# Performance work log

Measured on AMD Instinct MI355X. Metric: run time of the kernel, lower is better.

Reference implementation:

```python
import jax, jax.numpy as jnp
import numpy as np


def setup_inputs() -> dict:
    key = jax.random.key(0)
    k1, k2 = jax.random.split(key)
    B, S = 128, 131072
    x = jax.random.normal(k1, (B, S), dtype=jnp.float32)
    mask = jax.random.randint(k2, (B, S), 0, 2).astype(jnp.bool_)
    return {"x": x, "mask": mask}


def reference(x, mask):
    # Masked cumulative sum along dim=1: fused mask-multiply + prefix scan.
    return jnp.cumsum(x * mask.astype(x.dtype), axis=1)
```

## Files before the change

kernel.cpp:

```cpp
#include <hip/hip_runtime.h>


#define TPB 512
#define B_ROWS 128
#define S_LEN 131072
#define TILE 16384
#define TPR 8
#define NBLK 512
#define NWAVE 8
#define MAGIC 0x7F3A9C51u

typedef float f32x4 __attribute__((ext_vector_type(4)));

#define UNPACK_PR(rd, XV, MW)                                          \
    pr[rd][0] = (XV).x * (float)((MW) & 0xffu);                        \
    pr[rd][1] = pr[rd][0] + (XV).y * (float)(((MW) >> 8) & 0xffu);     \
    pr[rd][2] = pr[rd][1] + (XV).z * (float)(((MW) >> 16) & 0xffu);    \
    pr[rd][3] = pr[rd][2] + (XV).w * (float)((MW) >> 24);

#define MUL_PR_I(rd, XV, MI)                                           \
    pr[rd][0] = (XV).x * (float)(MI).x;                                \
    pr[rd][1] = pr[rd][0] + (XV).y * (float)(MI).y;                    \
    pr[rd][2] = pr[rd][1] + (XV).z * (float)(MI).z;                    \
    pr[rd][3] = pr[rd][2] + (XV).w * (float)(MI).w;

__device__ __forceinline__ void lds_barrier() {
    asm volatile("s_waitcnt lgkmcnt(0)" ::: "memory");
    __builtin_amdgcn_s_barrier();
}

__global__ void __launch_bounds__(TPB, 2)
mscan(const float* __restrict__ x, const void* __restrict__ mask,
      float* __restrict__ out, unsigned* __restrict__ ticket,
      unsigned long long* __restrict__ desc) {
    __shared__ unsigned s_vb;
    __shared__ float wtA[NWAVE], wtB[NWAVE];
    __shared__ float s_prevA;

    const int t = threadIdx.x;
    const int lane = t & 63, wid = t >> 6;

    if (t == 0) s_vb = atomicAdd(ticket, 1u) & (NBLK - 1);
    __syncthreads();
    const unsigned vb = s_vb;
    const int r = vb >> 2, q = vb & 3;
    const int tidA = r * TPR + 2 * q;
    const long eA = (long)r * S_LEN + (long)(2 * q) * TILE;
    const long eB = eA + TILE;

    const char* xbA  = (const char*)x + eA * 4 + wid * 8192 + lane * 16;
    const char* xbA2 = xbA + 4096;
    const char* mbA  = (const char*)mask + eA + wid * 2048 + lane * 4;
    const char* xbB  = (const char*)x + eB * 4 + wid * 8192 + lane * 16;
    const char* xbB2 = xbB + 4096;
    const char* mbB  = (const char*)mask + eB + wid * 2048 + lane * 4;
    const unsigned* dwp = (const unsigned*)mask + lane;

    unsigned dw;
    f32x4 x0, x1, x2, x3, x4v, x5, x6, x7;
    unsigned m0, m1, m2, m3, m4, m5, m6, m7;
    asm volatile(
        "global_load_dword %0, %17, off\n\t"
        "global_load_dwordx4 %1, %18, off\n\t"
        "global_load_dwordx4 %2, %18, off offset:1024\n\t"
        "global_load_dwordx4 %3, %18, off offset:2048\n\t"
        "global_load_dwordx4 %4, %18, off offset:3072\n\t"
        "global_load_dwordx4 %5, %19, off\n\t"
        "global_load_dwordx4 %6, %19, off offset:1024\n\t"
        "global_load_dwordx4 %7, %19, off offset:2048\n\t"
        "global_load_dwordx4 %8, %19, off offset:3072\n\t"
        "global_load_dword %9, %20, off\n\t"
        "global_load_dword %10, %20, off offset:256\n\t"
        "global_load_dword %11, %20, off offset:512\n\t"
        "global_load_dword %12, %20, off offset:768\n\t"
        "global_load_dword %13, %20, off offset:1024\n\t"
        "global_load_dword %14, %20, off offset:1280\n\t"
        "global_load_dword %15, %20, off offset:1536\n\t"
        "global_load_dword %16, %20, off offset:1792\n\t"
        "s_waitcnt vmcnt(0)"
        : "=&v"(dw), "=&v"(x0), "=&v"(x1), "=&v"(x2), "=&v"(x3),
          "=&v"(x4v), "=&v"(x5), "=&v"(x6), "=&v"(x7),
          "=&v"(m0), "=&v"(m1), "=&v"(m2), "=&v"(m3),
          "=&v"(m4), "=&v"(m5), "=&v"(m6), "=&v"(m7)
        : "v"(dwp), "v"(xbA), "v"(xbA2), "v"(mbA)
        : "memory");

    const bool m_i32 = (__all(dw <= 1u) != 0);

    float pr[8][4];
    f32x4 y0, y1, y2, y3, y4, y5, y6, y7;
    unsigned n0, n1, n2, n3, n4, n5, n6, n7;
    if (!m_i32) {
        UNPACK_PR(0, x0, m0)  UNPACK_PR(1, x1, m1)
        UNPACK_PR(2, x2, m2)  UNPACK_PR(3, x3, m3)
        UNPACK_PR(4, x4v, m4) UNPACK_PR(5, x5, m5)
        UNPACK_PR(6, x6, m6)  UNPACK_PR(7, x7, m7)
        asm volatile(
            "global_load_dwordx4 %0, %16, off\n\t"
            "global_load_dwordx4 %1, %16, off offset:1024\n\t"
            "global_load_dwordx4 %2, %16, off offset:2048\n\t"
            "global_load_dwordx4 %3, %16, off offset:3072\n\t"
            "global_load_dwordx4 %4, %17, off\n\t"
            "global_load_dwordx4 %5, %17, off offset:1024\n\t"
            "global_load_dwordx4 %6, %17, off offset:2048\n\t"
            "global_load_dwordx4 %7, %17, off offset:3072\n\t"
            "global_load_dword %8, %18, off\n\t"
            "global_load_dword %9, %18, off offset:256\n\t"
            "global_load_dword %10, %18, off offset:512\n\t"
            "global_load_dword %11, %18, off offset:768\n\t"
            "global_load_dword %12, %18, off offset:1024\n\t"
            "global_load_dword %13, %18, off offset:1280\n\t"
            "global_load_dword %14, %18, off offset:1536\n\t"
            "global_load_dword %15, %18, off offset:1792"
            : "=&v"(y0), "=&v"(y1), "=&v"(y2), "=&v"(y3),
              "=&v"(y4), "=&v"(y5), "=&v"(y6), "=&v"(y7),
              "=&v"(n0), "=&v"(n1), "=&v"(n2), "=&v"(n3),
              "=&v"(n4), "=&v"(n5), "=&v"(n6), "=&v"(n7)
            : "v"(xbB), "v"(xbB2), "v"(mbB)
            : "memory");
    } else {
        const char* mibA = (const char*)mask + eA * 4 + wid * 8192 + lane * 16;
        const int4 a0 = *(const int4*)(mibA + 0 * 1024);
        const int4 a1 = *(const int4*)(mibA + 1 * 1024);
        const int4 a2 = *(const int4*)(mibA + 2 * 1024);
        const int4 a3 = *(const int4*)(mibA + 3 * 1024);
        const int4 a4 = *(const int4*)(mibA + 4 * 1024);
        const int4 a5 = *(const int4*)(mibA + 5 * 1024);
        const int4 a6 = *(const int4*)(mibA + 6 * 1024);
        const int4 a7 = *(const int4*)(mibA + 7 * 1024);
        MUL_PR_I(0, x0, a0)  MUL_PR_I(1, x1, a1)
        MUL_PR_I(2, x2, a2)  MUL_PR_I(3, x3, a3)
        MUL_PR_I(4, x4v, a4) MUL_PR_I(5, x5, a5)
        MUL_PR_I(6, x6, a6)  MUL_PR_I(7, x7, a7)
    }

    float incA[8], rtA[8];
    #pragma unroll
    for (int rd = 0; rd < 8; ++rd) {
        float vv = pr[rd][3];
        #pragma unroll
        for (int off = 1; off < 64; off <<= 1) {
            const float n = __shfl_up(vv, off, 64);
            if (lane >= off) vv += n;
        }
        incA[rd] = vv;
        rtA[rd] = __shfl(vv, 63, 64);
    }
    float wsumA = 0.0f;
    #pragma unroll
    for (int rd = 0; rd < 8; ++rd) wsumA += rtA[rd];
    if (lane == 0) wtA[wid] = wsumA;
    lds_barrier();

    float wpreA = 0.0f, TA = 0.0f;
    #pragma unroll
    for (int w = 0; w < NWAVE; ++w) {
        const float qv = wtA[w];
        if (w < wid) wpreA += qv;
        TA += qv;
    }

    if (t == 0) {
        float prev = 0.0f;
        if (q != 0) {
            const unsigned long long* dp = &desc[tidA - 1];
            unsigned long long d;
            while (((d = __hip_atomic_load(dp, __ATOMIC_RELAXED,
                                           __HIP_MEMORY_SCOPE_AGENT)) >> 32)
                   != (unsigned long long)MAGIC)
                __builtin_amdgcn_s_sleep(2);
            union { unsigned u; float f; } cv; cv.u = (unsigned)d; prev = cv.f;
        }
        union { float f; unsigned u; } tv; tv.f = prev + TA;
        __hip_atomic_store(&desc[tidA],
                           ((unsigned long long)MAGIC << 32) | tv.u,
                           __ATOMIC_RELAXED, __HIP_MEMORY_SCOPE_AGENT);
        s_prevA = prev;
    }
    lds_barrier();
    const float prevA = s_prevA;

    {
        const float baseA = prevA + wpreA;
        char* ob = (char*)out + eA * 4 + wid * 8192 + lane * 16;
        float rpre = 0.0f;
        #pragma unroll
        for (int rd = 0; rd < 8; ++rd) {
            const float excl = baseA + rpre + (incA[rd] - pr[rd][3]);
            f32x4 ov;
            ov.x = excl + pr[rd][0];
            ov.y = excl + pr[rd][1];
            ov.z = excl + pr[rd][2];
            ov.w = excl + pr[rd][3];
            __builtin_nontemporal_store(ov, (f32x4*)(ob + rd * 1024));
            rpre += rtA[rd];
        }
    }

    if (!m_i32) {
        asm volatile("s_waitcnt vmcnt(8)" ::: "memory");
        __builtin_amdgcn_sched_barrier(0);
        UNPACK_PR(0, y0, n0)  UNPACK_PR(1, y1, n1)
        UNPACK_PR(2, y2, n2)  UNPACK_PR(3, y3, n3)
        UNPACK_PR(4, y4, n4)  UNPACK_PR(5, y5, n5)
        UNPACK_PR(6, y6, n6)  UNPACK_PR(7, y7, n7)
    } else {
        asm volatile("s_waitcnt vmcnt(0)" ::: "memory");
        __builtin_amdgcn_sched_barrier(0);
        const char* xib = (const char*)x + eB * 4 + wid * 8192 + lane * 16;
        const char* mib = (const char*)mask + eB * 4 + wid * 8192 + lane * 16;
        #pragma unroll
        for (int rd = 0; rd < 8; ++rd) {
            const f32x4 xv = *(const f32x4*)(xib + rd * 1024);
            const int4 mv = *(const int4*)(mib + rd * 1024);
            MUL_PR_I(rd, xv, mv)
        }
    }

    float incB[8], rtB[8];
    #pragma unroll
    for (int rd = 0; rd < 8; ++rd) {
        float vv = pr[rd][3];
        #pragma unroll
        for (int off = 1; off < 64; off <<= 1) {
            const float n = __shfl_up(vv, off, 64);
            if (lane >= off) vv += n;
        }
        incB[rd] = vv;
        rtB[rd] = __shfl(vv, 63, 64);
    }
    float wsumB = 0.0f;
    #pragma unroll
    for (int rd = 0; rd < 8; ++rd) wsumB += rtB[rd];
    if (lane == 0) wtB[wid] = wsumB;
    lds_barrier();

    float wpreB = 0.0f, TB = 0.0f;
    #pragma unroll
    for (int w = 0; w < NWAVE; ++w) {
        const float qv = wtB[w];
        if (w < wid) wpreB += qv;
        TB += qv;
    }
    const float prevB = prevA + TA;

    if (t == 0) {
        union { float f; unsigned u; } tv; tv.f = prevB + TB;
        __hip_atomic_store(&desc[tidA + 1],
                           ((unsigned long long)MAGIC << 32) | tv.u,
                           __ATOMIC_RELAXED, __HIP_MEMORY_SCOPE_AGENT);
    }

    {
        const float baseB = prevB + wpreB;
        char* ob = (char*)out + eB * 4 + wid * 8192 + lane * 16;
        float rpre = 0.0f;
        #pragma unroll
        for (int rd = 0; rd < 8; ++rd) {
            const float excl = baseB + rpre + (incB[rd] - pr[rd][3]);
            f32x4 ov;
            ov.x = excl + pr[rd][0];
            ov.y = excl + pr[rd][1];
            ov.z = excl + pr[rd][2];
            ov.w = excl + pr[rd][3];
            __builtin_nontemporal_store(ov, (f32x4*)(ob + rd * 1024));
            rpre += rtB[rd];
        }
    }
}

extern "C" void kernel_launch(void* const* d_in, const int* in_sizes, int n_in,
                              void* d_out, int out_size, void* d_ws, size_t ws_size,
                              hipStream_t stream) {
    const float* x    = (const float*)d_in[0];
    const void*  mask = d_in[1];
    float*       out  = (float*)d_out;

    unsigned* ticket         = (unsigned*)d_ws;
    unsigned long long* desc = (unsigned long long*)((char*)d_ws + 256);

    mscan<<<NBLK, TPB, 0, stream>>>(x, mask, out, ticket, desc);
}
```

Baseline: 41.08 us.

## Split each row into two 1024-thread blocks and hoist all tile loads upfront

Reorganizes the decoupled-lookback scan so each row is covered by two blocks of 1024 threads (256 blocks total) instead of four 512-thread blocks. Both sub-tiles' loads for x and the byte mask are now issued before any compute, rather than the second tile's loads waiting on the first. The lookback chain per row becomes a single dependency. The second-half block must wait for the first half's full total before storing anything, so more work sits on a serial dependency. Fewer blocks also lowers available parallelism and wave occupancy per CU.

After: 48.56 us. 1.18x slower.

```diff
diff --git a/kernel.cpp b/kernel.cpp
--- a/kernel.cpp
+++ b/kernel.cpp
@@ -1,13 +1,12 @@
 #include <hip/hip_runtime.h>
 
 
-#define TPB 512
+#define TPB 1024
+#define NWAVE 16
 #define B_ROWS 128
 #define S_LEN 131072
-#define TILE 16384
-#define TPR 8
-#define NBLK 512
-#define NWAVE 8
+#define SUB 32768
+#define NBLK 256
 #define MAGIC 0x7F3A9C51u
 
 typedef float f32x4 __attribute__((ext_vector_type(4)));
@@ -29,13 +28,49 @@
     __builtin_amdgcn_s_barrier();
 }
 
-__global__ void __launch_bounds__(TPB, 2)
+__device__ __forceinline__ float wave_scan8(const float (&pr)[8][4],
+                                            float (&inc)[8], float (&rt)[8],
+                                            const int lane) {
+    float tot = 0.0f;
+    #pragma unroll
+    for (int rd = 0; rd < 8; ++rd) {
+        float vv = pr[rd][3];
+        #pragma unroll
+        for (int off = 1; off < 64; off <<= 1) {
+            const float n = __shfl_up(vv, off, 64);
+            if (lane >= off) vv += n;
+        }
+        inc[rd] = vv;
+        rt[rd] = __shfl(vv, 63, 64);
+        tot += rt[rd];
+    }
+    return tot;
+}
+
+__device__ __forceinline__ void store8(const float (&pr)[8][4],
+                                       const float (&inc)[8], const float (&rt)[8],
+                                       const float base, char* ob) {
+    float rpre = 0.0f;
+    #pragma unroll
+    for (int rd = 0; rd < 8; ++rd) {
+        const float excl = base + rpre + (inc[rd] - pr[rd][3]);
+        f32x4 ov;
+        ov.x = excl + pr[rd][0];
+        ov.y = excl + pr[rd][1];
+        ov.z = excl + pr[rd][2];
+        ov.w = excl + pr[rd][3];
+        __builtin_nontemporal_store(ov, (f32x4*)(ob + rd * 1024));
+        rpre += rt[rd];
+    }
+}
+
+__global__ void __launch_bounds__(TPB)
 mscan(const float* __restrict__ x, const void* __restrict__ mask,
       float* __restrict__ out, unsigned* __restrict__ ticket,
       unsigned long long* __restrict__ desc) {
     __shared__ unsigned s_vb;
-    __shared__ float wtA[NWAVE], wtB[NWAVE];
-    __shared__ float s_prevA;
+    __shared__ float wt[NWAVE];
+    __shared__ float s_prev;
 
     const int t = threadIdx.x;
     const int lane = t & 63, wid = t >> 6;
@@ -43,17 +78,21 @@
     if (t == 0) s_vb = atomicAdd(ticket, 1u) & (NBLK - 1);
     __syncthreads();
     const unsigned vb = s_vb;
-    const int r = vb >> 2, q = vb & 3;
-    const int tidA = r * TPR + 2 * q;
-    const long eA = (long)r * S_LEN + (long)(2 * q) * TILE;
-    const long eB = eA + TILE;
-
-    const char* xbA  = (const char*)x + eA * 4 + wid * 8192 + lane * 16;
+    const int h = vb >> 7;
+    const int r = vb & (B_ROWS - 1);
+    const long eA = (long)r * S_LEN + (long)h * (2 * SUB);
+    const long eB = eA + SUB;
+
+    const int xoff = wid * 8192 + lane * 16;
+    const int moff = wid * 2048 + lane * 4;
+    const char* xw = (const char*)x;
+    const char* mw = (const char*)mask;
+    const char* xbA  = xw + eA * 4 + xoff;
     const char* xbA2 = xbA + 4096;
-    const char* mbA  = (const char*)mask + eA + wid * 2048 + lane * 4;
-    const char* xbB  = (const char*)x + eB * 4 + wid * 8192 + lane * 16;
+    const char* mbA  = mw + eA + moff;
+    const char* xbB  = xw + eB * 4 + xoff;
     const char* xbB2 = xbB + 4096;
-    const char* mbB  = (const char*)mask + eB + wid * 2048 + lane * 4;
+    const char* mbB  = mw + eB + moff;
     const unsigned* dwp = (const unsigned*)mask + lane;
 
     unsigned dw;
@@ -76,8 +115,7 @@
         "global_load_dword %13, %20, off offset:1024\n\t"
         "global_load_dword %14, %20, off offset:1280\n\t"
         "global_load_dword %15, %20, off offset:1536\n\t"
-        "global_load_dword %16, %20, off offset:1792\n\t"
-        "s_waitcnt vmcnt(0)"
+        "global_load_dword %16, %20, off offset:1792"
         : "=&v"(dw), "=&v"(x0), "=&v"(x1), "=&v"(x2), "=&v"(x3),
           "=&v"(x4v), "=&v"(x5), "=&v"(x6), "=&v"(x7),
           "=&v"(m0), "=&v"(m1), "=&v"(m2), "=&v"(m3),
@@ -85,85 +123,70 @@
         : "v"(dwp), "v"(xbA), "v"(xbA2), "v"(mbA)
         : "memory");
 
-    const bool m_i32 = (__all(dw <= 1u) != 0);
-
-    float pr[8][4];
     f32x4 y0, y1, y2, y3, y4, y5, y6, y7;
     unsigned n0, n1, n2, n3, n4, n5, n6, n7;
+    asm volatile(
+        "global_load_dwordx4 %0, %16, off\n\t"
+        "global_load_dwordx4 %1, %16, off offset:1024\n\t"
+        "global_load_dwordx4 %2, %16, off offset:2048\n\t"
+        "global_load_dwordx4 %3, %16, off offset:3072\n\t"
+        "global_load_dwordx4 %4, %17, off\n\t"
+        "global_load_dwordx4 %5, %17, off offset:1024\n\t"
+        "global_load_dwordx4 %6, %17, off offset:2048\n\t"
+        "global_load_dwordx4 %7, %17, off offset:3072\n\t"
+        "global_load_dword %8, %18, off\n\t"
+        "global_load_dword %9, %18, off offset:256\n\t"
+        "global_load_dword %10, %18, off offset:512\n\t"
+        "global_load_dword %11, %18, off offset:768\n\t"
+        "global_load_dword %12, %18, off offset:1024\n\t"
+        "global_load_dword %13, %18, off offset:1280\n\t"
+        "global_load_dword %14, %18, off offset:1536\n\t"
+        "global_load_dword %15, %18, off offset:1792"
+        : "=&v"(y0), "=&v"(y1), "=&v"(y2), "=&v"(y3),
+          "=&v"(y4), "=&v"(y5), "=&v"(y6), "=&v"(y7),
+          "=&v"(n0), "=&v"(n1), "=&v"(n2), "=&v"(n3),
+          "=&v"(n4), "=&v"(n5), "=&v"(n6), "=&v"(n7)
+        : "v"(xbB), "v"(xbB2), "v"(mbB)
+        : "memory");
+
+    asm volatile("s_waitcnt vmcnt(16)" ::: "memory");
+    __builtin_amdgcn_sched_barrier(0);
+    const bool m_i32 = (__all(dw <= 1u) != 0);
+
+    float pr[8][4];
     if (!m_i32) {
         UNPACK_PR(0, x0, m0)  UNPACK_PR(1, x1, m1)
         UNPACK_PR(2, x2, m2)  UNPACK_PR(3, x3, m3)
         UNPACK_PR(4, x4v, m4) UNPACK_PR(5, x5, m5)
         UNPACK_PR(6, x6, m6)  UNPACK_PR(7, x7, m7)
-        asm volatile(
-            "global_load_dwordx4 %0, %16, off\n\t"
-            "global_load_dwordx4 %1, %16, off offset:1024\n\t"
-            "global_load_dwordx4 %2, %16, off offset:2048\n\t"
-            "global_load_dwordx4 %3, %16, off offset:3072\n\t"
-            "global_load_dwordx4 %4, %17, off\n\t"
-            "global_load_dwordx4 %5, %17, off offset:1024\n\t"
-            "global_load_dwordx4 %6, %17, off offset:2048\n\t"
-            "global_load_dwordx4 %7, %17, off offset:3072\n\t"
-            "global_load_dword %8, %18, off\n\t"
-            "global_load_dword %9, %18, off offset:256\n\t"
-            "global_load_dword %10, %18, off offset:512\n\t"
-            "global_load_dword %11, %18, off offset:768\n\t"
-            "global_load_dword %12, %18, off offset:1024\n\t"
-            "global_load_dword %13, %18, off offset:1280\n\t"
-            "global_load_dword %14, %18, off offset:1536\n\t"
-            "global_load_dword %15, %18, off offset:1792"
-            : "=&v"(y0), "=&v"(y1), "=&v"(y2), "=&v"(y3),
-              "=&v"(y4), "=&v"(y5), "=&v"(y6), "=&v"(y7),
-              "=&v"(n0), "=&v"(n1), "=&v"(n2), "=&v"(n3),
-              "=&v"(n4), "=&v"(n5), "=&v"(n6), "=&v"(n7)
-            : "v"(xbB), "v"(xbB2), "v"(mbB)
-            : "memory");
     } else {
-        const char* mibA = (const char*)mask + eA * 4 + wid * 8192 + lane * 16;
-        const int4 a0 = *(const int4*)(mibA + 0 * 1024);
-        const int4 a1 = *(const int4*)(mibA + 1 * 1024);
-        const int4 a2 = *(const int4*)(mibA + 2 * 1024);
-        const int4 a3 = *(const int4*)(mibA + 3 * 1024);
-        const int4 a4 = *(const int4*)(mibA + 4 * 1024);
-        const int4 a5 = *(const int4*)(mibA + 5 * 1024);
-        const int4 a6 = *(const int4*)(mibA + 6 * 1024);
-        const int4 a7 = *(const int4*)(mibA + 7 * 1024);
-        MUL_PR_I(0, x0, a0)  MUL_PR_I(1, x1, a1)
-        MUL_PR_I(2, x2, a2)  MUL_PR_I(3, x3, a3)
-        MUL_PR_I(4, x4v, a4) MUL_PR_I(5, x5, a5)
-        MUL_PR_I(6, x6, a6)  MUL_PR_I(7, x7, a7)
-    }
-
-    float incA[8], rtA[8];
-    #pragma unroll
-    for (int rd = 0; rd < 8; ++rd) {
-        float vv = pr[rd][3];
+        asm volatile("s_waitcnt vmcnt(0)" ::: "memory");
+        __builtin_amdgcn_sched_barrier(0);
+        const char* mib = mw + eA * 4 + xoff;
         #pragma unroll
-        for (int off = 1; off < 64; off <<= 1) {
-            const float n = __shfl_up(vv, off, 64);
-            if (lane >= off) vv += n;
-        }
-        incA[rd] = vv;
-        rtA[rd] = __shfl(vv, 63, 64);
-    }
-    float wsumA = 0.0f;
-    #pragma unroll
-    for (int rd = 0; rd < 8; ++rd) wsumA += rtA[rd];
-    if (lane == 0) wtA[wid] = wsumA;
-    lds_barrier();
-
+        for (int rd = 0; rd < 8; ++rd) {
+            const f32x4 xv = *(const f32x4*)(xw + eA * 4 + xoff + rd * 1024);
+            const int4 mv = *(const int4*)(mib + rd * 1024);
+            MUL_PR_I(rd, xv, mv)
+        }
+    }
+
+    float inc[8], rt[8];
+    const float wavetotA = wave_scan8(pr, inc, rt, lane);
+    if (lane == 0) wt[wid] = wavetotA;
+    lds_barrier();
     float wpreA = 0.0f, TA = 0.0f;
     #pragma unroll
     for (int w = 0; w < NWAVE; ++w) {
-        const float qv = wtA[w];
+        const float qv = wt[w];
         if (w < wid) wpreA += qv;
         TA += qv;
     }
 
     if (t == 0) {
         float prev = 0.0f;
-        if (q != 0) {
-            const unsigned long long* dp = &desc[tidA - 1];
+        if (h != 0) {
+            const unsigned long long* dp = &desc[r];
             unsigned long long d;
             while (((d = __hip_atomic_load(dp, __ATOMIC_RELAXED,
                                            __HIP_MEMORY_SCOPE_AGENT)) >> 32)
@@ -171,31 +194,12 @@
                 __builtin_amdgcn_s_sleep(2);
             union { unsigned u; float f; } cv; cv.u = (unsigned)d; prev = cv.f;
         }
-        union { float f; unsigned u; } tv; tv.f = prev + TA;
-        __hip_atomic_store(&desc[tidA],
-                           ((unsigned long long)MAGIC << 32) | tv.u,
-                           __ATOMIC_RELAXED, __HIP_MEMORY_SCOPE_AGENT);
-        s_prevA = prev;
-    }
-    lds_barrier();
-    const float prevA = s_prevA;
-
-    {
-        const float baseA = prevA + wpreA;
-        char* ob = (char*)out + eA * 4 + wid * 8192 + lane * 16;
-        float rpre = 0.0f;
-        #pragma unroll
-        for (int rd = 0; rd < 8; ++rd) {
-            const float excl = baseA + rpre + (incA[rd] - pr[rd][3]);
-            f32x4 ov;
-            ov.x = excl + pr[rd][0];
-            ov.y = excl + pr[rd][1];
-            ov.z = excl + pr[rd][2];
-            ov.w = excl + pr[rd][3];
-            __builtin_nontemporal_store(ov, (f32x4*)(ob + rd * 1024));
-            rpre += rtA[rd];
-        }
-    }
+        s_prev = prev;
+    }
+    lds_barrier();
+    const float prev = s_prev;
+
+    store8(pr, inc, rt, prev + wpreA, (char*)out + eA * 4 + xoff);
 
     if (!m_i32) {
         asm volatile("s_waitcnt vmcnt(8)" ::: "memory");
@@ -205,68 +209,35 @@
         UNPACK_PR(4, y4, n4)  UNPACK_PR(5, y5, n5)
         UNPACK_PR(6, y6, n6)  UNPACK_PR(7, y7, n7)
     } else {
-        asm volatile("s_waitcnt vmcnt(0)" ::: "memory");
-        __builtin_amdgcn_sched_barrier(0);
-        const char* xib = (const char*)x + eB * 4 + wid * 8192 + lane * 16;
-        const char* mib = (const char*)mask + eB * 4 + wid * 8192 + lane * 16;
+        const char* mib = mw + eB * 4 + xoff;
         #pragma unroll
         for (int rd = 0; rd < 8; ++rd) {
-            const f32x4 xv = *(const f32x4*)(xib + rd * 1024);
+            const f32x4 xv = *(const f32x4*)(xw + eB * 4 + xoff + rd * 1024);
             const int4 mv = *(const int4*)(mib + rd * 1024);
             MUL_PR_I(rd, xv, mv)
         }
     }
 
-    float incB[8], rtB[8];
-    #pragma unroll
-    for (int rd = 0; rd < 8; ++rd) {
-        float vv = pr[rd][3];
-        #pragma unroll
-        for (int off = 1; off < 64; off <<= 1) {
-            const float n = __shfl_up(vv, off, 64);
-            if (lane >= off) vv += n;
-        }
-        incB[rd] = vv;
-        rtB[rd] = __shfl(vv, 63, 64);
-    }
-    float wsumB = 0.0f;
-    #pragma unroll
-    for (int rd = 0; rd < 8; ++rd) wsumB += rtB[rd];
-    if (lane == 0) wtB[wid] = wsumB;
-    lds_barrier();
-
+    const float wavetotB = wave_scan8(pr, inc, rt, lane);
+    lds_barrier();
+    if (lane == 0) wt[wid] = wavetotB;
+    lds_barrier();
     float wpreB = 0.0f, TB = 0.0f;
     #pragma unroll
     for (int w = 0; w < NWAVE; ++w) {
-        const float qv = wtB[w];
+        const float qv = wt[w];
         if (w < wid) wpreB += qv;
         TB += qv;
     }
-    const float prevB = prevA + TA;
-
-    if (t == 0) {
-        union { float f; unsigned u; } tv; tv.f = prevB + TB;
-        __hip_atomic_store(&desc[tidA + 1],
+
+    if (h == 0 && t == 0) {
+        union { float f; unsigned u; } tv; tv.f = TA + TB;
+        __hip_atomic_store(&desc[r],
                            ((unsigned long long)MAGIC << 32) | tv.u,
                            __ATOMIC_RELAXED, __HIP_MEMORY_SCOPE_AGENT);
     }
 
-    {
-        const float baseB = prevB + wpreB;
-        char* ob = (char*)out + eB * 4 + wid * 8192 + lane * 16;
-        float rpre = 0.0f;
-        #pragma unroll
-        for (int rd = 0; rd < 8; ++rd) {
-            const float excl = baseB + rpre + (incB[rd] - pr[rd][3]);
-            f32x4 ov;
-            ov.x = excl + pr[rd][0];
-            ov.y = excl + pr[rd][1];
-            ov.z = excl + pr[rd][2];
-            ov.w = excl + pr[rd][3];
-            __builtin_nontemporal_store(ov, (f32x4*)(ob + rd * 1024));
-            rpre += rtB[rd];
-        }
-    }
+    store8(pr, inc, rt, prev + TA + wpreB, (char*)out + eB * 4 + xoff);
 }
 
 extern "C" void kernel_launch(void* const* d_in, const int* in_sizes, int n_in,
```
